# Kernel tuning notes

Measured on AMD Instinct MI355X. Metric: run time of the kernel, lower is better.

## Reference

```python
import jax, jax.numpy as jnp
from jax import lax
import numpy as np

B, S, I, H, L, D = 64, 1024, 512, 512, 2, 2  # batch, seq, input, hidden, layers, directions


def setup_inputs() -> dict:
    key = jax.random.key(0)
    ks = jax.random.split(key, 6)
    scale = 0.05  # keep gates out of saturation (torch code uses raw randn; scaled for numerics)
    return {
        "x": jax.random.normal(ks[0], (B, S, I), jnp.float32),
        "Wi": jax.random.normal(ks[1], (L, D, 3, I, H), jnp.float32) * scale,  # gates: [r, z, n]
        "Wh": jax.random.normal(ks[2], (L, D, 3, H, H), jnp.float32) * scale,
        "b": jax.random.normal(ks[3], (L, D, 3, H), jnp.float32) * scale,
        "fc_w": jax.random.normal(ks[4], (D * H, H), jnp.float32) * scale,
        "fc_b": jax.random.normal(ks[5], (H,), jnp.float32) * scale,
    }


def _run_layer(x_seq, wi, wh, bb):
    """One GRU layer, one direction. x_seq: [B,S,Hin]; wi/wh: [3,Hin,H]; bb: [3,H]."""
    batch = x_seq.shape[0]
    h_dim = wh.shape[-1]
    # Precompute all input projections (+biases) once: [S, 3, B, H]
    xs = jnp.einsum('bsi,gih->sgbh', x_seq, wi) + bb[None, :, None, :]

    def step(h, xg):
        r = jax.nn.sigmoid(xg[0] + h @ wh[0])
        z = jax.nn.sigmoid(xg[1] + h @ wh[1])
        n = jnp.tanh(xg[2] + r * (h @ wh[2]))
        h_next = (1.0 - z) * n + z * h
        return h_next, h_next

    h0 = jnp.zeros((batch, h_dim), x_seq.dtype)
    _, ys = lax.scan(step, h0, xs)  # ys: [S, B, H]
    return ys.transpose(1, 0, 2)  # [B, S, H]


def reference(x, Wi, Wh, b, fc_w, fc_b):
    n_layers = Wi.shape[0]
    # forward direction: stack layers, feed layer output as next layer input
    out_f = x
    for l in range(n_layers):
        out_f = _run_layer(out_f, Wi[l, 0], Wh[l, 0], b[l, 0])
    # backward direction: process time-reversed sequence, then flip back
    out_b = x[:, ::-1, :]
    for l in range(n_layers):
        out_b = _run_layer(out_b, Wi[l, 1], Wh[l, 1], b[l, 1])
    out_b = out_b[:, ::-1, :]
    outputs = jnp.concatenate([out_f, out_b], axis=2)  # [B, S, 2H]
    return outputs[:, -1, :] @ fc_w + fc_b  # [B, H]
```

## Files before the change

### kernel.cpp

```cpp
#include <hip/hip_runtime.h>
#include <cstdint>
#include <cmath>


typedef __attribute__((ext_vector_type(8))) short bf16x8;
typedef __attribute__((ext_vector_type(4))) float f32x4;
typedef __attribute__((ext_vector_type(4))) unsigned int u32x4;

#define DEV static __device__ __forceinline__

DEV unsigned short f2bf(float f) {
  union { float f; uint32_t u; } v; v.f = f;
  uint32_t u = v.u;
  return (unsigned short)((u + (((u >> 16) & 1u) + 0x7fffu)) >> 16);
}
DEV float bf2f(unsigned short h) {
  union { uint32_t u; float f; } v; v.u = ((uint32_t)h) << 16;
  return v.f;
}
DEV float fsig(float x)  { return 1.f / (1.f + __expf(-x)); }
DEV float ftanh(float x) { return 2.f / (1.f + __expf(-2.f * x)) - 1.f; }

static constexpr int Ss = 1024, Ii = 512;

static constexpr size_t WIMG_PER_LS = 131072;
static constexpr size_t OFF_WIMG = 0;
static constexpr size_t WIMG_BYTES = (size_t)64 * WIMG_PER_LS;
static constexpr size_t OFF_H1  = OFF_WIMG + WIMG_BYTES;
static constexpr size_t OFF_H2  = OFF_H1 + 524288;
static constexpr size_t OFF_FLG = OFF_H2 + 524288;
static constexpr size_t OFF_H2F = OFF_FLG + 4096;
static constexpr size_t OFF_HB1 = OFF_H2F + 131072;
static constexpr size_t OFF_HB2 = OFF_HB1 + 131072;
static constexpr size_t WS_NEED = OFF_HB2 + 131072;

__global__ __launch_bounds__(256) void prep_weights(const float* __restrict__ Wi,
                                                    const float* __restrict__ Wh,
                                                    unsigned short* __restrict__ img) {
  uint32_t idx = blockIdx.x * 256 + threadIdx.x;
  uint32_t ls = idx >> 16;
  uint32_t off = idx & 65535u;
  int l = (int)(ls >> 5), s = (int)(ls & 31);
  int m, g, cc, kg, kr;
  bool lo = off >= 49152u;
  if (!lo) {
    m = (int)(off / 24576u); uint32_t r = off % 24576u;
    kg = (int)(r / 384u); r %= 384u;
    int c = (int)(r >> 3); kr = (int)(r & 7u);
    g = c >> 4; cc = c & 15;
  } else {
    uint32_t o2 = off - 49152u;
    m = (int)(o2 >> 13); uint32_t r = o2 & 8191u;
    kg = (int)(r >> 7); r &= 127u;
    cc = (int)(r >> 3); kr = (int)(r & 7u);
    g = 2;
  }
  int h = s * 16 + cc, k = kg * 8 + kr;
  const float* W = m ? Wh : Wi;
  float v = W[((size_t)(l * 6 + g) * 512 + k) * 512 + h];
  unsigned short hv = f2bf(v);
  if (lo) hv = f2bf(v - bf2f(hv));
  img[(size_t)ls * 65536 + off] = hv;
}

__global__ __launch_bounds__(256) void init_state(uint32_t* __restrict__ hz,
                                                  int* __restrict__ flg) {
  int tid = blockIdx.x * 256 + threadIdx.x;
  if (tid < 262144) hz[tid] = 0u;
  if (tid < 1024) flg[tid] = ((tid & 15) == 0 && tid >= 512) ? 1 : 0;
}

#define MFMA(AA, BB, CC) CC = __builtin_amdgcn_mfma_f32_16x16x32_bf16(AA, BB, CC, 0, 0, 0)
#define SB0 __builtin_amdgcn_sched_barrier(0)
#define VMWAIT0 asm volatile("s_waitcnt vmcnt(0)" ::: "memory")
#define VMWAIT8 asm volatile("s_waitcnt vmcnt(8)" ::: "memory")
#define LD16CP(dst, addr) \
  asm volatile("global_load_dwordx4 %0, %1, off sc0 sc1" : "=&v"(dst) : "v"((const void*)(addr)))
#define ST2CP(addr, val) \
  asm volatile("global_store_short %0, %1, off sc0 sc1" :: "v"((void*)(addr)), "v"((uint32_t)(val)) : "memory")
#define ST4CP(addr, val) \
  asm volatile("global_store_dword %0, %1, off sc0 sc1" :: "v"((void*)(addr)), "v"(val) : "memory")

DEV int pollcp(const int* p) {
  int v;
  asm volatile("global_load_dword %0, %1, off sc0 sc1\ns_waitcnt vmcnt(0)"
               : "=v"(v) : "v"((const void*)p) : "memory");
  return v;
}

DEV void wait_combined(int* flg, int tgtA, int tgtB, int lane, int& alive) {
  const int* p = flg + lane * 16;
  const int tgt = (lane < 32) ? tgtA : tgtB;
  const int lim = alive ? (1 << 17) : 64;
  int spins = 0;
  for (;;) {
    int v = pollcp(p);
    if (__all(v >= tgt)) break;
    __builtin_amdgcn_s_sleep(1);
    if (++spins > lim) { alive = 0; break; }
  }
}

#define ISSUE8(R, ABASE, BOFF)                                                 \
  _Pragma("unroll")                                                            \
  for (int j = 0; j < 4; ++j) {                                                \
    LD16CP(R[2*j],   (ABASE) + (BOFF) + 64 * j);                               \
    LD16CP(R[2*j+1], (ABASE) + (BOFF) + 64 * j + 65536);                       \
  }
#define MFB_REG(R, b, A0, A1, A2)                                              \
  _Pragma("unroll")                                                            \
  for (int j = 0; j < 4; ++j) {                                                \
    const int kk = 4 * (b) + j;                                                \
    const int kg = 16 * (b) + 4 * j + q;                                       \
    bf16x8 ql = *(const bf16x8*)(lds + 98304 + 16384 + (size_t)kg * 256 + (size_t)l15 * 16); \
    MFMA(R[2*j], hB[kk*3+0], A0); MFMA(R[2*j+1], hB[kk*3+0], A0);              \
    MFMA(R[2*j], hB[kk*3+1], A1); MFMA(R[2*j+1], hB[kk*3+1], A1);              \
    MFMA(R[2*j], hB[kk*3+2], A2); MFMA(R[2*j+1], hB[kk*3+2], A2);              \
    MFMA(R[2*j], ql, A2);                                                      \
  }
#define MFB_LDSB(R, b, A0, A1, A2)                                             \
  _Pragma("unroll")                                                            \
  for (int j = 0; j < 4; ++j) {                                                \
    const int kg = 16 * (b) + 4 * j + q;                                       \
    const unsigned char* wb = lds + (size_t)kg * 768 + (size_t)l15 * 16;       \
    bf16x8 q0 = *(const bf16x8*)(wb);                                          \
    bf16x8 q1 = *(const bf16x8*)(wb + 256);                                    \
    bf16x8 q2 = *(const bf16x8*)(wb + 512);                                    \
    bf16x8 ql = *(const bf16x8*)(lds + 98304 + (size_t)kg * 256 + (size_t)l15 * 16); \
    MFMA(R[2*j], q0, A0); MFMA(R[2*j+1], q0, A0);                              \
    MFMA(R[2*j], q1, A1); MFMA(R[2*j+1], q1, A1);                              \
    MFMA(R[2*j], q2, A2); MFMA(R[2*j+1], q2, A2);                              \
    MFMA(R[2*j], ql, A2);                                                      \
  }
#define HGEMM(ABASE, MFB, A0, A1, A2)                                          \
  {                                                                            \
    bf16x8 fa[8], fb[8];                                                       \
    SB0; ISSUE8(fa, ABASE, 0)  SB0; ISSUE8(fb, ABASE, 256) SB0;                \
    VMWAIT8; SB0; MFB(fa, 0, A0, A1, A2) SB0;                                  \
    ISSUE8(fa, ABASE, 512) SB0; VMWAIT8; SB0; MFB(fb, 1, A0, A1, A2) SB0;      \
    ISSUE8(fb, ABASE, 768) SB0; VMWAIT8; SB0; MFB(fa, 2, A0, A1, A2) SB0;      \
    VMWAIT0; SB0; MFB(fb, 3, A0, A1, A2) SB0;                                  \
  }
#define XGEMM(T0)                                                              \
  {                                                                            \
    const float* xr = xr0 + (size_t)(T0) * Ii;                                 \
    _Pragma("unroll 4")                                                        \
    for (int kk = 0; kk < 16; ++kk) {                                          \
      const int kg = kk * 4 + q;                                               \
      f32x4 va = *(const f32x4*)(xr + kg * 8);                                 \
      f32x4 vb = *(const f32x4*)(xr + kg * 8 + 4);                             \
      bf16x8 ahi, alo;                                                         \
      _Pragma("unroll")                                                        \
      for (int e = 0; e < 4; ++e) {                                            \
        unsigned short ha = f2bf(va[e]);                                       \
        ((unsigned short*)&ahi)[e] = ha;                                       \
        ((unsigned short*)&alo)[e] = f2bf(va[e] - bf2f(ha));                   \
        unsigned short hb_ = f2bf(vb[e]);                                      \
        ((unsigned short*)&ahi)[e + 4] = hb_;                                  \
        ((unsigned short*)&alo)[e + 4] = f2bf(vb[e] - bf2f(hb_));              \
      }                                                                        \
      const unsigned char* wb = lds + (size_t)kg * 768 + (size_t)l15 * 16;     \
      bf16x8 q0 = *(const bf16x8*)(wb);                                        \
      bf16x8 q1 = *(const bf16x8*)(wb + 256);                                  \
      bf16x8 q2 = *(const bf16x8*)(wb + 512);                                  \
      bf16x8 ql = *(const bf16x8*)(lds + 98304 + (size_t)kg * 256 + (size_t)l15 * 16); \
      MFMA(ahi, q0, ax0); MFMA(alo, q0, ax0);                                  \
      MFMA(ahi, q1, ax1); MFMA(alo, q1, ax1);                                  \
      MFMA(ahi, q2, ax2); MFMA(alo, q2, ax2);                                  \
      MFMA(ahi, ql, ax2);                                                      \
    }                                                                          \
  }

__global__ __launch_bounds__(256, 1) void gru_persistent(const float* __restrict__ x,
                                                         const float* __restrict__ bias,
                                                         unsigned char* __restrict__ ws) {
  __shared__ unsigned char lds[131072];
  const int tid = threadIdx.x, lane = tid & 63, wv = tid >> 6;
  const int bid = blockIdx.x;
  const int xcd = bid & 7;
  const int layer = xcd >> 2;
  const int slice = (xcd & 3) * 8 + (bid >> 3);
  const int l15 = lane & 15, q = lane >> 4;

  {
    const u32x4* src = (const u32x4*)(ws + OFF_WIMG + (size_t)(layer * 32 + slice) * WIMG_PER_LS);
    u32x4* dst = (u32x4*)lds;
    for (int i = tid; i < 8192; i += 256) dst[i] = src[i];
  }
  __syncthreads();

  bf16x8 hB[48];
#pragma unroll
  for (int kk = 0; kk < 16; ++kk) {
    const int kg = kk * 4 + q;
    const unsigned char* wb = lds + 49152 + (size_t)kg * 768 + (size_t)l15 * 16;
    hB[kk * 3 + 0] = *(const bf16x8*)(wb);
    hB[kk * 3 + 1] = *(const bf16x8*)(wb + 256);
    hB[kk * 3 + 2] = *(const bf16x8*)(wb + 512);
  }

  unsigned char* h1b = ws + OFF_H1;
  unsigned char* h2b = ws + OFF_H2;
  int* flg = (int*)(ws + OFF_FLG);
  float* h2f = (float*)(ws + OFF_H2F);

  const int colg = slice * 16 + l15;
  const int row0 = wv * 16 + q * 4;
  const int arow = wv * 16 + l15;
  const float b0 = bias[(size_t)(layer * 6 + 0) * 512 + colg];
  const float b1 = bias[(size_t)(layer * 6 + 1) * 512 + colg];
  const float b2 = bias[(size_t)(layer * 6 + 2) * 512 + colg];

  int* myflag = flg + (layer * 32 + slice) * 16;
  f32x4 hprev{0.f, 0.f, 0.f, 0.f};
  int alive = 1;

  if (layer == 0) {
    const float* xr0 = x + (size_t)arow * Ss * Ii;
    f32x4 ax0{}, ax1{}, ax2{};
    XGEMM(0)
    for (int T = 1; T <= 1024; ++T) {
      if (wv == 0) wait_combined(flg, T - 1, T - 3, lane, alive);
      __syncthreads();
      f32x4 ah0{}, ah1{}, ah2{};
      const unsigned char* ab = h1b + (size_t)((T - 1) & 3) * 131072 + (size_t)arow * 1024 + (size_t)q * 16;
      HGEMM(ab, MFB_REG, ah0, ah1, ah2)
      unsigned char* hd = h1b + (size_t)(T & 3) * 131072;
#pragma unroll
      for (int e = 0; e < 4; ++e) {
        float rr = fsig(ax0[e] + ah0[e] + b0);
        float zz = fsig(ax1[e] + ah1[e] + b1);
        float nn = ftanh(ax2[e] + b2 + rr * ah2[e]);
        float hn = (1.f - zz) * nn + zz * hprev[e];
        hprev[e] = hn;
        unsigned short hi = f2bf(hn), lo = f2bf(hn - bf2f(hi));
        size_t ob = (size_t)(row0 + e) * 1024 + (size_t)colg * 2;
        ST2CP(hd + ob, hi); ST2CP(hd + ob + 65536, lo);
      }
      VMWAIT0;
      __syncthreads();
      if (tid == 0) ST4CP(myflag, T);
      ax0 = f32x4{}; ax1 = f32x4{}; ax2 = f32x4{};
      if (T < 1024) XGEMM(T)
    }
  } else {
    for (int T = 2; T <= 1025; ++T) {
      if (wv == 0) wait_combined(flg, T - 1, T - 1, lane, alive);
      __syncthreads();
      f32x4 ax0{}, ax1{}, ax2{}, ah0{}, ah1{}, ah2{};
      const unsigned char* ab2 = h2b + (size_t)((T - 2) & 3) * 131072 + (size_t)arow * 1024 + (size_t)q * 16;
      HGEMM(ab2, MFB_REG, ah0, ah1, ah2)
      const unsigned char* ab1 = h1b + (size_t)((T - 1) & 3) * 131072 + (size_t)arow * 1024 + (size_t)q * 16;
      HGEMM(ab1, MFB_LDSB, ax0, ax1, ax2)
      unsigned char* hd = h2b + (size_t)((T - 1) & 3) * 131072;
#pragma unroll
      for (int e = 0; e < 4; ++e) {
        float rr = fsig(ax0[e] + ah0[e] + b0);
        float zz = fsig(ax1[e] + ah1[e] + b1);
        float nn = ftanh(ax2[e] + b2 + rr * ah2[e]);
        float hn = (1.f - zz) * nn + zz * hprev[e];
        hprev[e] = hn;
        unsigned short hi = f2bf(hn), lo = f2bf(hn - bf2f(hi));
        size_t ob = (size_t)(row0 + e) * 1024 + (size_t)colg * 2;
        ST2CP(hd + ob, hi); ST2CP(hd + ob + 65536, lo);
        if (T == 1025) h2f[(size_t)(row0 + e) * 512 + colg] = hn;
      }
      VMWAIT0;
      __syncthreads();
      if (tid == 0) ST4CP(myflag, T);
    }
  }
}

__global__ __launch_bounds__(256) void gru_bstep(const float* __restrict__ inp, long rstride,
                                                 const float* __restrict__ Wi,
                                                 const float* __restrict__ bias,
                                                 float* __restrict__ out) {
  __shared__ float a[8192];
  int tid = threadIdx.x;
  int bg = blockIdx.x >> 4, cg = blockIdx.x & 15;
  for (int j = 0; j < 32; ++j) {
    int idx = j * 256 + tid;
    int r = idx >> 9, k = idx & 511;
    a[idx] = inp[(size_t)(bg * 16 + r) * rstride + k];
  }
  __syncthreads();
  int col = cg * 32 + (tid & 31);
  int r0 = tid >> 5;
  float z0 = bias[512 + col], z1 = z0;
  float n0 = bias[1024 + col], n1 = n0;
  const float* W1 = Wi + (size_t)512 * 512;
  const float* W2 = Wi + (size_t)2 * 512 * 512;
  for (int k = 0; k < 512; ++k) {
    float wz = W1[(size_t)k * 512 + col];
    float wn = W2[(size_t)k * 512 + col];
    float a0 = a[r0 * 512 + k], a1 = a[(r0 + 8) * 512 + k];
    z0 += a0 * wz; z1 += a1 * wz;
    n0 += a0 * wn; n1 += a1 * wn;
  }
  float s0 = fsig(z0), s1 = fsig(z1);
  out[(size_t)(bg * 16 + r0) * 512 + col]     = (1.f - s0) * ftanh(n0);
  out[(size_t)(bg * 16 + r0 + 8) * 512 + col] = (1.f - s1) * ftanh(n1);
}

__global__ __launch_bounds__(256) void fc_kernel(const float* __restrict__ h2f,
                                                 const float* __restrict__ hb2,
                                                 const float* __restrict__ fcw,
                                                 const float* __restrict__ fcb,
                                                 float* __restrict__ out) {
  __shared__ float a[16384];
  int tid = threadIdx.x;
  int bg = blockIdx.x >> 4, cg = blockIdx.x & 15;
  for (int j = 0; j < 32; ++j) {
    int idx = j * 256 + tid;
    int r = idx >> 9, k = idx & 511;
    a[r * 1024 + k]       = h2f[(size_t)(bg * 16 + r) * 512 + k];
    a[r * 1024 + 512 + k] = hb2[(size_t)(bg * 16 + r) * 512 + k];
  }
  __syncthreads();
  int col = cg * 32 + (tid & 31);
  int r0 = tid >> 5;
  float s0 = fcb[col], s1 = fcb[col];
  for (int k = 0; k < 1024; ++k) {
    float wvv = fcw[(size_t)k * 512 + col];
    s0 += a[r0 * 1024 + k] * wvv;
    s1 += a[(r0 + 8) * 1024 + k] * wvv;
  }
  out[(size_t)(bg * 16 + r0) * 512 + col]     = s0;
  out[(size_t)(bg * 16 + r0 + 8) * 512 + col] = s1;
}

extern "C" void kernel_launch(void* const* d_in, const int* in_sizes, int n_in,
                              void* d_out, int out_size, void* d_ws, size_t ws_size,
                              hipStream_t stream) {
  const float* x   = (const float*)d_in[0];
  const float* Wi  = (const float*)d_in[1];
  const float* Wh  = (const float*)d_in[2];
  const float* b   = (const float*)d_in[3];
  const float* fcw = (const float*)d_in[4];
  const float* fcb = (const float*)d_in[5];
  float* out = (float*)d_out;
  unsigned char* ws = (unsigned char*)d_ws;
  if (ws_size < WS_NEED) return;

  prep_weights<<<16384, 256, 0, stream>>>(Wi, Wh, (unsigned short*)(ws + OFF_WIMG));
  init_state<<<1024, 256, 0, stream>>>((uint32_t*)(ws + OFF_H1), (int*)(ws + OFF_FLG));
  gru_persistent<<<64, 256, 0, stream>>>(x, b, ws);
  gru_bstep<<<64, 256, 0, stream>>>(x + (size_t)1023 * 512, (long)Ss * Ii,
                                    Wi + (size_t)3 * 512 * 512, b + 3 * 512,
                                    (float*)(ws + OFF_HB1));
  gru_bstep<<<64, 256, 0, stream>>>((const float*)(ws + OFF_HB1), 512L,
                                    Wi + (size_t)9 * 512 * 512, b + 9 * 512,
                                    (float*)(ws + OFF_HB2));
  fc_kernel<<<64, 256, 0, stream>>>((const float*)(ws + OFF_H2F), (const float*)(ws + OFF_HB2),
                                    fcw, fcb, out);
}
```

Before: 13.74 ms.

## Move layer-1 input projection into layer-0 blocks via global staging buffer

```diff
diff --git a/kernel.cpp b/kernel.cpp
--- a/kernel.cpp
+++ b/kernel.cpp
@@ -29,7 +29,8 @@
 static constexpr size_t OFF_H1  = OFF_WIMG + WIMG_BYTES;
 static constexpr size_t OFF_H2  = OFF_H1 + 524288;
 static constexpr size_t OFF_FLG = OFF_H2 + 524288;
-static constexpr size_t OFF_H2F = OFF_FLG + 4096;
+static constexpr size_t OFF_XG  = OFF_FLG + 4096;
+static constexpr size_t OFF_H2F = OFF_XG + 1572864;
 static constexpr size_t OFF_HB1 = OFF_H2F + 131072;
 static constexpr size_t OFF_HB2 = OFF_HB1 + 131072;
 static constexpr size_t WS_NEED = OFF_HB2 + 131072;
@@ -76,6 +77,8 @@
 #define VMWAIT8 asm volatile("s_waitcnt vmcnt(8)" ::: "memory")
 #define LD16CP(dst, addr) \
   asm volatile("global_load_dwordx4 %0, %1, off sc0 sc1" : "=&v"(dst) : "v"((const void*)(addr)))
+#define LD4CPF(dst, addr) \
+  asm volatile("global_load_dword %0, %1, off sc0 sc1" : "=&v"(dst) : "v"((const void*)(addr)))
 #define ST2CP(addr, val) \
   asm volatile("global_store_short %0, %1, off sc0 sc1" :: "v"((void*)(addr)), "v"((uint32_t)(val)) : "memory")
 #define ST4CP(addr, val) \
@@ -112,25 +115,31 @@
   for (int j = 0; j < 4; ++j) {                                                \
     const int kk = 4 * (b) + j;                                                \
     const int kg = 16 * (b) + 4 * j + q;                                       \
-    bf16x8 ql = *(const bf16x8*)(lds + 98304 + 16384 + (size_t)kg * 256 + (size_t)l15 * 16); \
+    bf16x8 ql = *(const bf16x8*)(lds + 114688 + (size_t)kg * 256 + (size_t)l15 * 16); \
     MFMA(R[2*j], hB[kk*3+0], A0); MFMA(R[2*j+1], hB[kk*3+0], A0);              \
     MFMA(R[2*j], hB[kk*3+1], A1); MFMA(R[2*j+1], hB[kk*3+1], A1);              \
     MFMA(R[2*j], hB[kk*3+2], A2); MFMA(R[2*j+1], hB[kk*3+2], A2);              \
     MFMA(R[2*j], ql, A2);                                                      \
   }
-#define MFB_LDSB(R, b, A0, A1, A2)                                             \
+#define MFB_DUAL(R, b)                                                         \
   _Pragma("unroll")                                                            \
   for (int j = 0; j < 4; ++j) {                                                \
+    const int kk = 4 * (b) + j;                                                \
     const int kg = 16 * (b) + 4 * j + q;                                       \
-    const unsigned char* wb = lds + (size_t)kg * 768 + (size_t)l15 * 16;       \
-    bf16x8 q0 = *(const bf16x8*)(wb);                                          \
-    bf16x8 q1 = *(const bf16x8*)(wb + 256);                                    \
-    bf16x8 q2 = *(const bf16x8*)(wb + 512);                                    \
-    bf16x8 ql = *(const bf16x8*)(lds + 98304 + (size_t)kg * 256 + (size_t)l15 * 16); \
-    MFMA(R[2*j], q0, A0); MFMA(R[2*j+1], q0, A0);                              \
-    MFMA(R[2*j], q1, A1); MFMA(R[2*j+1], q1, A1);                              \
-    MFMA(R[2*j], q2, A2); MFMA(R[2*j+1], q2, A2);                              \
-    MFMA(R[2*j], ql, A2);                                                      \
+    bf16x8 qlh = *(const bf16x8*)(lds + 114688 + (size_t)kg * 256 + (size_t)l15 * 16); \
+    MFMA(R[2*j], hB[kk*3+0], ah0); MFMA(R[2*j+1], hB[kk*3+0], ah0);            \
+    MFMA(R[2*j], hB[kk*3+1], ah1); MFMA(R[2*j+1], hB[kk*3+1], ah1);            \
+    MFMA(R[2*j], hB[kk*3+2], ah2); MFMA(R[2*j+1], hB[kk*3+2], ah2);            \
+    MFMA(R[2*j], qlh, ah2);                                                    \
+    const unsigned char* wb2 = lds + 49152 + (size_t)kg * 768 + (size_t)l15 * 16; \
+    bf16x8 p0 = *(const bf16x8*)(wb2);                                         \
+    bf16x8 p1 = *(const bf16x8*)(wb2 + 256);                                   \
+    bf16x8 p2 = *(const bf16x8*)(wb2 + 512);                                   \
+    bf16x8 qli = *(const bf16x8*)(lds + 131072 + (size_t)kg * 256 + (size_t)l15 * 16); \
+    MFMA(R[2*j], p0, bx0); MFMA(R[2*j+1], p0, bx0);                            \
+    MFMA(R[2*j], p1, bx1); MFMA(R[2*j+1], p1, bx1);                            \
+    MFMA(R[2*j], p2, bx2); MFMA(R[2*j+1], p2, bx2);                            \
+    MFMA(R[2*j], qli, bx2);                                                    \
   }
 #define HGEMM(ABASE, MFB, A0, A1, A2)                                          \
   {                                                                            \
@@ -140,6 +149,15 @@
     ISSUE8(fa, ABASE, 512) SB0; VMWAIT8; SB0; MFB(fb, 1, A0, A1, A2) SB0;      \
     ISSUE8(fb, ABASE, 768) SB0; VMWAIT8; SB0; MFB(fa, 2, A0, A1, A2) SB0;      \
     VMWAIT0; SB0; MFB(fb, 3, A0, A1, A2) SB0;                                  \
+  }
+#define HGEMM_DUAL(ABASE)                                                      \
+  {                                                                            \
+    bf16x8 fa[8], fb[8];                                                       \
+    SB0; ISSUE8(fa, ABASE, 0)  SB0; ISSUE8(fb, ABASE, 256) SB0;                \
+    VMWAIT8; SB0; MFB_DUAL(fa, 0) SB0;                                         \
+    ISSUE8(fa, ABASE, 512) SB0; VMWAIT8; SB0; MFB_DUAL(fb, 1) SB0;             \
+    ISSUE8(fb, ABASE, 768) SB0; VMWAIT8; SB0; MFB_DUAL(fa, 2) SB0;             \
+    VMWAIT0; SB0; MFB_DUAL(fb, 3) SB0;                                         \
   }
 #define XGEMM(T0)                                                              \
   {                                                                            \
@@ -174,7 +192,7 @@
 __global__ __launch_bounds__(256, 1) void gru_persistent(const float* __restrict__ x,
                                                          const float* __restrict__ bias,
                                                          unsigned char* __restrict__ ws) {
-  __shared__ unsigned char lds[131072];
+  __shared__ unsigned char lds[147456];
   const int tid = threadIdx.x, lane = tid & 63, wv = tid >> 6;
   const int bid = blockIdx.x;
   const int xcd = bid & 7;
@@ -198,6 +216,14 @@
     hB[kk * 3 + 1] = *(const bf16x8*)(wb + 256);
     hB[kk * 3 + 2] = *(const bf16x8*)(wb + 512);
   }
+  __syncthreads();
+  if (layer == 0) {
+    const u32x4* src2 = (const u32x4*)(ws + OFF_WIMG + (size_t)(32 + slice) * WIMG_PER_LS);
+    u32x4* dst = (u32x4*)lds;
+    for (int i = tid; i < 3072; i += 256) dst[3072 + i] = src2[i];
+    for (int i = tid; i < 1024; i += 256) dst[8192 + i] = src2[6144 + i];
+  }
+  __syncthreads();
 
   unsigned char* h1b = ws + OFF_H1;
   unsigned char* h2b = ws + OFF_H2;
@@ -219,45 +245,66 @@
     const float* xr0 = x + (size_t)arow * Ss * Ii;
     f32x4 ax0{}, ax1{}, ax2{};
     XGEMM(0)
-    for (int T = 1; T <= 1024; ++T) {
+    for (int T = 1; T <= 1025; ++T) {
       if (wv == 0) wait_combined(flg, T - 1, T - 3, lane, alive);
       __syncthreads();
-      f32x4 ah0{}, ah1{}, ah2{};
+      f32x4 ah0{}, ah1{}, ah2{}, bx0{}, bx1{}, bx2{};
       const unsigned char* ab = h1b + (size_t)((T - 1) & 3) * 131072 + (size_t)arow * 1024 + (size_t)q * 16;
-      HGEMM(ab, MFB_REG, ah0, ah1, ah2)
-      unsigned char* hd = h1b + (size_t)(T & 3) * 131072;
+      HGEMM_DUAL(ab)
+      float* xgp = (float*)(ws + OFF_XG + (size_t)((T - 1) & 3) * 393216 + (size_t)slice * 12288);
+      if (T <= 1024) {
+        unsigned char* hd = h1b + (size_t)(T & 3) * 131072;
+#pragma unroll
+        for (int e = 0; e < 4; ++e) {
+          float rr = fsig(ax0[e] + ah0[e] + b0);
+          float zz = fsig(ax1[e] + ah1[e] + b1);
+          float nn = ftanh(ax2[e] + b2 + rr * ah2[e]);
+          float hn = (1.f - zz) * nn + zz * hprev[e];
+          hprev[e] = hn;
+          unsigned short hi = f2bf(hn), lo = f2bf(hn - bf2f(hi));
+          size_t ob = (size_t)(row0 + e) * 1024 + (size_t)colg * 2;
+          ST2CP(hd + ob, hi); ST2CP(hd + ob + 65536, lo);
+        }
+      }
 #pragma unroll
       for (int e = 0; e < 4; ++e) {
-        float rr = fsig(ax0[e] + ah0[e] + b0);
-        float zz = fsig(ax1[e] + ah1[e] + b1);
-        float nn = ftanh(ax2[e] + b2 + rr * ah2[e]);
-        float hn = (1.f - zz) * nn + zz * hprev[e];
-        hprev[e] = hn;
-        unsigned short hi = f2bf(hn), lo = f2bf(hn - bf2f(hi));
-        size_t ob = (size_t)(row0 + e) * 1024 + (size_t)colg * 2;
-        ST2CP(hd + ob, hi); ST2CP(hd + ob + 65536, lo);
+        float* xp = xgp + (size_t)(row0 + e) * 48 + l15;
+        ST4CP(xp,      bx0[e]);
+        ST4CP(xp + 16, bx1[e]);
+        ST4CP(xp + 32, bx2[e]);
       }
       VMWAIT0;
       __syncthreads();
       if (tid == 0) ST4CP(myflag, T);
-      ax0 = f32x4{}; ax1 = f32x4{}; ax2 = f32x4{};
-      if (T < 1024) XGEMM(T)
+      if (T < 1024) {
+        ax0 = f32x4{}; ax1 = f32x4{}; ax2 = f32x4{};
+        XGEMM(T)
+      }
     }
   } else {
     for (int T = 2; T <= 1025; ++T) {
-      if (wv == 0) wait_combined(flg, T - 1, T - 1, lane, alive);
+      if (wv == 0) wait_combined(flg, T, T - 1, lane, alive);
       __syncthreads();
-      f32x4 ax0{}, ax1{}, ax2{}, ah0{}, ah1{}, ah2{};
+      f32x4 ah0{}, ah1{}, ah2{};
       const unsigned char* ab2 = h2b + (size_t)((T - 2) & 3) * 131072 + (size_t)arow * 1024 + (size_t)q * 16;
       HGEMM(ab2, MFB_REG, ah0, ah1, ah2)
-      const unsigned char* ab1 = h1b + (size_t)((T - 1) & 3) * 131072 + (size_t)arow * 1024 + (size_t)q * 16;
-      HGEMM(ab1, MFB_LDSB, ax0, ax1, ax2)
+      const float* xgp = (const float*)(ws + OFF_XG + (size_t)((T - 1) & 3) * 393216 + (size_t)slice * 12288);
+      float xf[12];
+      SB0;
+#pragma unroll
+      for (int e = 0; e < 4; ++e) {
+        const float* xp = xgp + (size_t)(row0 + e) * 48 + l15;
+        LD4CPF(xf[e * 3 + 0], xp);
+        LD4CPF(xf[e * 3 + 1], xp + 16);
+        LD4CPF(xf[e * 3 + 2], xp + 32);
+      }
+      VMWAIT0; SB0;
       unsigned char* hd = h2b + (size_t)((T - 1) & 3) * 131072;
 #pragma unroll
       for (int e = 0; e < 4; ++e) {
-        float rr = fsig(ax0[e] + ah0[e] + b0);
-        float zz = fsig(ax1[e] + ah1[e] + b1);
-        float nn = ftanh(ax2[e] + b2 + rr * ah2[e]);
+        float rr = fsig(xf[e * 3 + 0] + ah0[e] + b0);
+        float zz = fsig(xf[e * 3 + 1] + ah1[e] + b1);
+        float nn = ftanh(xf[e * 3 + 2] + b2 + rr * ah2[e]);
         float hn = (1.f - zz) * nn + zz * hprev[e];
         hprev[e] = hn;
         unsigned short hi = f2bf(hn), lo = f2bf(hn - bf2f(hi));
```

After: 14.39 ms. +4.7%, slower.
